# Kernel optimization log

Hardware: AMD Instinct MI355X
Metric: run time of the kernel (lower is better)

Reference implementation:

```python
import jax, jax.numpy as jnp
import numpy as np
from jax import lax

B, SEQ, D, DEPTH = 256, 50, 256, 4
N, K, R = 16, 4, 16  # d_state, d_conv, dt_rank
EPS = 1e-5


def rmsnorm(x, w):
    var = jnp.mean(jnp.square(x), axis=-1, keepdims=True)
    return x * lax.rsqrt(var + EPS) * w


def mamba_mixer(h, in_proj_w, conv_w, conv_b, x_proj_w, dt_proj_w, dt_proj_b, A_log, D_skip, out_proj_w):
    # h: (B, L, D)
    xz = h @ in_proj_w                       # (B, L, 2D)
    x_in, z = jnp.split(xz, 2, axis=-1)      # each (B, L, D)
    # causal depthwise conv1d, kernel K, groups=D
    x_bdl = x_in.transpose(0, 2, 1)          # (B, D, L)
    kern = conv_w[:, None, :]                # (D, 1, K)
    x_c = lax.conv_general_dilated(x_bdl, kern, window_strides=(1,),
                                   padding=[(K - 1, 0)], feature_group_count=D,
                                   dimension_numbers=('NCH', 'OIH', 'NCH'))
    x_c = jax.nn.silu(x_c + conv_b[None, :, None]).transpose(0, 2, 1)  # (B, L, D)
    # input-dependent SSM params
    x_dbl = x_c @ x_proj_w                   # (B, L, R+2N)
    dt = jax.nn.softplus(x_dbl[..., :R] @ dt_proj_w + dt_proj_b)       # (B, L, D)
    Bm = x_dbl[..., R:R + N]                 # (B, L, N)
    Cm = x_dbl[..., R + N:]                  # (B, L, N)
    A = -jnp.exp(A_log)                      # (D, N)
    dA = jnp.exp(dt[..., None] * A)          # (B, L, D, N)
    dBx = (dt * x_c)[..., None] * Bm[:, :, None, :]                    # (B, L, D, N)

    def step(hstate, inp):
        dA_t, dBx_t, C_t = inp
        hstate = dA_t * hstate + dBx_t      # (B, D, N)
        y_t = jnp.einsum('bdn,bn->bd', hstate, C_t)
        return hstate, y_t

    h0 = jnp.zeros((h.shape[0], D, N), dtype=h.dtype)
    xs = (dA.transpose(1, 0, 2, 3), dBx.transpose(1, 0, 2, 3), Cm.transpose(1, 0, 2))
    _, ys = lax.scan(step, h0, xs)           # (L, B, D)
    y = ys.transpose(1, 0, 2) + D_skip * x_c
    y = y * jax.nn.silu(z)
    return y @ out_proj_w                    # (B, L, D)


def setup_inputs() -> dict:
    key = jax.random.key(0)
    ks = jax.random.split(key, 16)
    sc = lambda *s: 0.02
    inp = {
        'x': jax.random.normal(ks[0], (B, SEQ), dtype=jnp.float32),
        'proj_w': jax.random.normal(ks[1], (1, D), dtype=jnp.float32) * 0.5,
        'proj_b': jnp.zeros((D,), dtype=jnp.float32),
        'cls_token': jax.random.normal(ks[2], (1, 1, D), dtype=jnp.float32) * 0.02,
        'pos_embed': jax.random.normal(ks[3], (1, SEQ + 1, D), dtype=jnp.float32) * 0.02,
        'norm_w': jnp.ones((DEPTH, D), dtype=jnp.float32),
        'in_proj_w': jax.random.normal(ks[4], (DEPTH, D, 2 * D), dtype=jnp.float32) * (D ** -0.5),
        'conv_w': jax.random.normal(ks[5], (DEPTH, D, K), dtype=jnp.float32) * 0.3,
        'conv_b': jnp.zeros((DEPTH, D), dtype=jnp.float32),
        'x_proj_w': jax.random.normal(ks[6], (DEPTH, D, R + 2 * N), dtype=jnp.float32) * (D ** -0.5),
        'dt_proj_w': jax.random.normal(ks[7], (DEPTH, R, D), dtype=jnp.float32) * (R ** -0.5),
        'dt_proj_b': jnp.log(jnp.expm1(jnp.full((DEPTH, D), 0.01, dtype=jnp.float32))),
        'A_log': jnp.broadcast_to(jnp.log(jnp.arange(1, N + 1, dtype=jnp.float32)), (DEPTH, D, N)).copy(),
        'D_skip': jnp.ones((DEPTH, D), dtype=jnp.float32),
        'out_proj_w': jax.random.normal(ks[8], (DEPTH, D, D), dtype=jnp.float32) * (D ** -0.5),
        'norm_f_w': jnp.ones((D,), dtype=jnp.float32),
    }
    return inp


def reference(x, proj_w, proj_b, cls_token, pos_embed, norm_w, in_proj_w, conv_w,
              conv_b, x_proj_w, dt_proj_w, dt_proj_b, A_log, D_skip, out_proj_w, norm_f_w):
    # LinearEmbed: (B, SEQ) -> (B, SEQ, 1) -> (B, SEQ, D)
    h = x[..., None] @ proj_w + proj_b
    h = h + pos_embed[:, :-1, :]
    cls = cls_token + pos_embed[:, -1:, :]
    h = jnp.concatenate([jnp.broadcast_to(cls, (h.shape[0], 1, D)), h], axis=1)  # (B, L=51, D)
    residual = None
    for i in range(DEPTH):
        residual = h if residual is None else residual + h
        hn = rmsnorm(residual, norm_w[i])
        h = mamba_mixer(hn, in_proj_w[i], conv_w[i], conv_b[i], x_proj_w[i],
                        dt_proj_w[i], dt_proj_b[i], A_log[i], D_skip[i], out_proj_w[i])
    out = rmsnorm(h, norm_f_w)
    return out[:, 0, :]  # return_type='cls'
```

## Files before the change

### kernel.cpp

```cpp
#include <hip/hip_runtime.h>
#include <math.h>

#define DD 256
#define DEPTH 4
#define XD 48
#define NBLK 16
#define NTHR 256


__device__ __forceinline__ float llc_loadf(const float* p) {
    return __hip_atomic_load(p, __ATOMIC_RELAXED, __HIP_MEMORY_SCOPE_AGENT);
}
__device__ __forceinline__ void llc_storef(float* p, float v) {
    __hip_atomic_store(p, v, __ATOMIC_RELAXED, __HIP_MEMORY_SCOPE_AGENT);
}

__device__ __forceinline__ void grid_bar(unsigned int* cnt, unsigned int target) {
    __syncthreads();
    if (threadIdx.x == 0) {
        __hip_atomic_fetch_add(cnt, 1u, __ATOMIC_RELAXED, __HIP_MEMORY_SCOPE_AGENT);
        while (__hip_atomic_load(cnt, __ATOMIC_RELAXED, __HIP_MEMORY_SCOPE_AGENT) < target)
            __builtin_amdgcn_s_sleep(1);
    }
    __syncthreads();
}

__global__ void netmamba_init(unsigned int* cnt) { *cnt = 0u; }

__global__ __launch_bounds__(NTHR, 1)
void netmamba_persist(const float* __restrict__ cls_token,
                      const float* __restrict__ pos_embed,
                      const float* __restrict__ norm_w,
                      const float* __restrict__ in_proj_w,
                      const float* __restrict__ conv_w,
                      const float* __restrict__ conv_b,
                      const float* __restrict__ x_proj_w,
                      const float* __restrict__ dt_proj_w,
                      const float* __restrict__ dt_proj_b,
                      const float* __restrict__ D_skip,
                      const float* __restrict__ out_proj_w,
                      const float* __restrict__ norm_f_w,
                      float* __restrict__ out,
                      float* __restrict__ ws)
{
    const int tid = threadIdx.x, bid = blockIdx.x;
    float* xc_g = ws;
    float* zv_g = ws + DD;
    float* hv_g = ws + 2 * DD;
    unsigned int* cnt = (unsigned int*)(ws + 1024);

    __shared__ float hn[DD], xcl[DD], yv[DD], xdbl[XD];
    __shared__ float4 partA[32][8];
    __shared__ float4 partB[64][4];
    __shared__ float xp[XD][4];
    __shared__ float red[4];
    __shared__ float rstd_s;

    float res_reg = 0.f;
    unsigned int phase = 0;

    for (int L = 0; L < DEPTH; ++L) {
        float rn;
        if (L == 0) rn = cls_token[tid] + pos_embed[50 * DD + tid];
        else        rn = res_reg + llc_loadf(&hv_g[tid]);
        res_reg = rn;

        float ss = rn * rn;
        #pragma unroll
        for (int o = 32; o > 0; o >>= 1) ss += __shfl_down(ss, o, 64);
        if ((tid & 63) == 0) red[tid >> 6] = ss;
        __syncthreads();
        if (tid == 0)
            rstd_s = rsqrtf((red[0] + red[1] + red[2] + red[3]) * (1.f / DD) + 1e-5f);
        __syncthreads();
        hn[tid] = rn * rstd_s * norm_w[L * DD + tid];
        __syncthreads();

        {
            const float4* W4 = (const float4*)in_proj_w + (size_t)L * DD * 128;
            const int cg = tid & 7, seg = tid >> 3;
            const int col4 = bid * 8 + cg;
            float4 acc = make_float4(0.f, 0.f, 0.f, 0.f);
            #pragma unroll
            for (int i = 0; i < 8; ++i) {
                const int d = seg * 8 + i;
                const float h = hn[d];
                const float4 w = W4[(size_t)d * 128 + col4];
                acc.x += h * w.x; acc.y += h * w.y;
                acc.z += h * w.z; acc.w += h * w.w;
            }
            partA[seg][cg] = acc;
        }
        __syncthreads();
        if (tid < 32) {
            const float* pf = (const float*)partA;
            float s = 0.f;
            #pragma unroll
            for (int g = 0; g < 32; ++g) s += pf[g * 32 + tid];
            const int gc = bid * 32 + tid;
            if (gc < DD) {
                const float pre = conv_w[(L * DD + gc) * 4 + 3] * s + conv_b[L * DD + gc];
                llc_storef(&xc_g[gc], pre / (1.f + __expf(-pre)));
            } else {
                llc_storef(&zv_g[gc - DD], s);
            }
        }
        ++phase;
        grid_bar(cnt, phase * NBLK);

        xcl[tid] = llc_loadf(&xc_g[tid]);
        const float zval = llc_loadf(&zv_g[tid]);
        __syncthreads();

        if (tid < 192) {
            const int j = tid >> 2, q = tid & 3;
            const float* Wx = x_proj_w + (size_t)L * DD * XD;
            float acc = 0.f;
            #pragma unroll 8
            for (int i = 0; i < 64; ++i) {
                const int d = q * 64 + i;
                acc += xcl[d] * Wx[(size_t)d * XD + j];
            }
            xp[j][q] = acc;
        }
        __syncthreads();
        if (tid < XD) xdbl[tid] = xp[tid][0] + xp[tid][1] + xp[tid][2] + xp[tid][3];
        __syncthreads();

        {
            const float* Wdt = dt_proj_w + (size_t)L * 16 * DD;
            float acc = dt_proj_b[L * DD + tid];
            #pragma unroll
            for (int r = 0; r < 16; ++r) acc += xdbl[r] * Wdt[r * DD + tid];
            const float dtv = fmaxf(acc, 0.f) + log1pf(__expf(-fabsf(acc)));
            float sbc = 0.f;
            #pragma unroll
            for (int n = 0; n < 16; ++n) sbc += xdbl[16 + n] * xdbl[32 + n];
            const float y = (dtv * sbc + D_skip[L * DD + tid]) * xcl[tid];
            yv[tid] = y * (zval / (1.f + __expf(-zval)));
        }
        __syncthreads();

        {
            const float4* Wo = (const float4*)out_proj_w + (size_t)L * DD * 64;
            const int c = tid & 3, seg = tid >> 2;
            const int col4 = bid * 4 + c;
            float4 acc = make_float4(0.f, 0.f, 0.f, 0.f);
            #pragma unroll
            for (int i = 0; i < 4; ++i) {
                const int d = seg * 4 + i;
                const float y = yv[d];
                const float4 w = Wo[(size_t)d * 64 + col4];
                acc.x += y * w.x; acc.y += y * w.y;
                acc.z += y * w.z; acc.w += y * w.w;
            }
            partB[seg][c] = acc;
        }
        __syncthreads();
        #pragma unroll
        for (int off = 32; off >= 8; off >>= 1) {
            const int s = tid >> 2, c = tid & 3;
            if (s < off) {
                float4 a = partB[s][c], b = partB[s + off][c];
                a.x += b.x; a.y += b.y; a.z += b.z; a.w += b.w;
                partB[s][c] = a;
            }
            __syncthreads();
        }
        if (tid < 16) {
            const float* pf = (const float*)partB;
            float s = 0.f;
            #pragma unroll
            for (int g = 0; g < 8; ++g) s += pf[g * 16 + tid];
            llc_storef(&hv_g[bid * 16 + tid], s);
        }
        ++phase;
        grid_bar(cnt, phase * NBLK);
    }

    {
        const float x = llc_loadf(&hv_g[tid]);
        float ss = x * x;
        #pragma unroll
        for (int o = 32; o > 0; o >>= 1) ss += __shfl_down(ss, o, 64);
        if ((tid & 63) == 0) red[tid >> 6] = ss;
        __syncthreads();
        if (tid == 0)
            rstd_s = rsqrtf((red[0] + red[1] + red[2] + red[3]) * (1.f / DD) + 1e-5f);
        __syncthreads();
        hn[tid] = x * rstd_s * norm_f_w[tid];
    }
    __syncthreads();
    {
        const float4* o4 = (const float4*)hn;
        float4* out4 = (float4*)out;
        #pragma unroll
        for (int k = 0; k < 4; ++k) {
            const int idx = k * NTHR + tid;
            const int row = bid * 16 + (idx >> 6);
            out4[(size_t)row * 64 + (idx & 63)] = o4[idx & 63];
        }
    }
}

extern "C" void kernel_launch(void* const* d_in, const int* in_sizes, int n_in,
                              void* d_out, int out_size, void* d_ws, size_t ws_size,
                              hipStream_t stream) {
    float* ws = (float*)d_ws;
    unsigned int* cnt = (unsigned int*)(ws + 1024);

    netmamba_init<<<dim3(1), dim3(1), 0, stream>>>(cnt);
    netmamba_persist<<<dim3(NBLK), dim3(NTHR), 0, stream>>>(
        (const float*)d_in[3], (const float*)d_in[4], (const float*)d_in[5],
        (const float*)d_in[6], (const float*)d_in[7], (const float*)d_in[8],
        (const float*)d_in[9], (const float*)d_in[10], (const float*)d_in[11],
        (const float*)d_in[13], (const float*)d_in[14], (const float*)d_in[15],
        (float*)d_out, ws);
}
```

Baseline: 44.11 us.

## Restructure into per-layer dataflow blocks with preloaded weights and point-to-point flags

```diff
diff --git a/kernel.cpp b/kernel.cpp
--- a/kernel.cpp
+++ b/kernel.cpp
@@ -3,10 +3,22 @@
 
 #define DD 256
 #define DEPTH 4
-#define XD 48
-#define NBLK 16
+#define WPG 16
+#define BPG 17
+#define NBLK (DEPTH * BPG)
 #define NTHR 256
 
+#define WS_XC   0
+#define WS_ZV   256
+#define WS_YV   512
+#define WS_HV   1024
+#define WS_FLAG 2048
+
+#define NX_WX   0
+#define NX_WDT  13312
+#define NX_DS   17408
+#define NX_DB   17664
+#define DYN_FLOATS 17920
 
 __device__ __forceinline__ float llc_loadf(const float* p) {
     return __hip_atomic_load(p, __ATOMIC_RELAXED, __HIP_MEMORY_SCOPE_AGENT);
@@ -14,56 +26,103 @@
 __device__ __forceinline__ void llc_storef(float* p, float v) {
     __hip_atomic_store(p, v, __ATOMIC_RELAXED, __HIP_MEMORY_SCOPE_AGENT);
 }
-
-__device__ __forceinline__ void grid_bar(unsigned int* cnt, unsigned int target) {
-    __syncthreads();
-    if (threadIdx.x == 0) {
-        __hip_atomic_fetch_add(cnt, 1u, __ATOMIC_RELAXED, __HIP_MEMORY_SCOPE_AGENT);
-        while (__hip_atomic_load(cnt, __ATOMIC_RELAXED, __HIP_MEMORY_SCOPE_AGENT) < target)
-            __builtin_amdgcn_s_sleep(1);
-    }
-    __syncthreads();
-}
-
-__global__ void netmamba_init(unsigned int* cnt) { *cnt = 0u; }
+__device__ __forceinline__ unsigned llc_loadu(const unsigned* p) {
+    return __hip_atomic_load(p, __ATOMIC_RELAXED, __HIP_MEMORY_SCOPE_AGENT);
+}
+__device__ __forceinline__ void flag_add(unsigned* p) {
+    __hip_atomic_fetch_add(p, 1u, __ATOMIC_RELAXED, __HIP_MEMORY_SCOPE_AGENT);
+}
+
+__global__ void netmamba_init(unsigned* flags) { flags[threadIdx.x] = 0u; }
 
 __global__ __launch_bounds__(NTHR, 1)
-void netmamba_persist(const float* __restrict__ cls_token,
-                      const float* __restrict__ pos_embed,
-                      const float* __restrict__ norm_w,
-                      const float* __restrict__ in_proj_w,
-                      const float* __restrict__ conv_w,
-                      const float* __restrict__ conv_b,
-                      const float* __restrict__ x_proj_w,
-                      const float* __restrict__ dt_proj_w,
-                      const float* __restrict__ dt_proj_b,
-                      const float* __restrict__ D_skip,
-                      const float* __restrict__ out_proj_w,
-                      const float* __restrict__ norm_f_w,
-                      float* __restrict__ out,
-                      float* __restrict__ ws)
+void netmamba_df(const float* __restrict__ cls_token,
+                 const float* __restrict__ pos_embed,
+                 const float* __restrict__ norm_w,
+                 const float* __restrict__ in_proj_w,
+                 const float* __restrict__ conv_w,
+                 const float* __restrict__ conv_b,
+                 const float* __restrict__ x_proj_w,
+                 const float* __restrict__ dt_proj_w,
+                 const float* __restrict__ dt_proj_b,
+                 const float* __restrict__ D_skip,
+                 const float* __restrict__ out_proj_w,
+                 const float* __restrict__ norm_f_w,
+                 float* __restrict__ out,
+                 float* __restrict__ ws)
 {
-    const int tid = threadIdx.x, bid = blockIdx.x;
-    float* xc_g = ws;
-    float* zv_g = ws + DD;
-    float* hv_g = ws + 2 * DD;
-    unsigned int* cnt = (unsigned int*)(ws + 1024);
-
-    __shared__ float hn[DD], xcl[DD], yv[DD], xdbl[XD];
-    __shared__ float4 partA[32][8];
-    __shared__ float4 partB[64][4];
-    __shared__ float xp[XD][4];
+    extern __shared__ float dyn[];
+    const int tid = threadIdx.x;
+    const int bid = blockIdx.x;
+    const int g   = bid / BPG;
+    const int r   = bid % BPG;
+    const bool narrow = (r == WPG);
+
+    float* xc_g = ws + WS_XC;
+    float* zv_g = ws + WS_ZV;
+    float* yv_g = ws + WS_YV;
+    float* hv_g = ws + WS_HV;
+    unsigned* flags = (unsigned*)(ws + WS_FLAG);
+
+    __shared__ float sh_a[DD];
+    __shared__ float sh_b[DD];
+    __shared__ float sh_c[DD];
+    __shared__ float sh_d[64];
     __shared__ float red[4];
     __shared__ float rstd_s;
 
-    float res_reg = 0.f;
-    unsigned int phase = 0;
-
-    for (int L = 0; L < DEPTH; ++L) {
-        float rn;
-        if (L == 0) rn = cls_token[tid] + pos_embed[50 * DD + tid];
-        else        rn = res_reg + llc_loadf(&hv_g[tid]);
-        res_reg = rn;
+    if (!narrow) {
+        const float4* Gi = (const float4*)in_proj_w + (size_t)(g * DD) * 128 + r * 8;
+        float4* Li = (float4*)dyn;
+        #pragma unroll
+        for (int k = 0; k < 8; ++k) {
+            const int m = tid + k * 256;
+            Li[m] = Gi[(size_t)(m >> 3) * 128 + (m & 7)];
+        }
+        const float4* Go = (const float4*)out_proj_w + (size_t)(g * DD) * 64 + r * 4;
+        float4* Lo = (float4*)(dyn + 8192);
+        #pragma unroll
+        for (int k = 0; k < 4; ++k) {
+            const int m = tid + k * 256;
+            Lo[m] = Go[(size_t)(m >> 2) * 64 + (m & 3)];
+        }
+        if (r < 8 && tid < 32) {
+            const int gc = r * 32 + tid;
+            sh_d[tid]      = conv_w[((size_t)g * DD + gc) * 4 + 3];
+            sh_d[32 + tid] = conv_b[g * DD + gc];
+        }
+    } else {
+        const float4* Gx = (const float4*)x_proj_w + (size_t)(g * DD) * 12;
+        #pragma unroll
+        for (int k = 0; k < 12; ++k) {
+            const int m = tid + k * 256;
+            const int d = m / 12, c4 = m % 12;
+            *(float4*)(dyn + NX_WX + d * 52 + c4 * 4) = Gx[(size_t)d * 12 + c4];
+        }
+        const float4* Gd = (const float4*)dt_proj_w + (size_t)g * 1024;
+        float4* Ld = (float4*)(dyn + NX_WDT);
+        #pragma unroll
+        for (int k = 0; k < 4; ++k) { const int m = tid + k * 256; Ld[m] = Gd[m]; }
+        dyn[NX_DS + tid] = D_skip[g * DD + tid];
+        dyn[NX_DB + tid] = dt_proj_b[g * DD + tid];
+    }
+    const float nf_reg = norm_f_w[tid];
+    float iv_reg = 0.f, nw_reg = 0.f;
+    if (!narrow) {
+        iv_reg = cls_token[tid] + pos_embed[50 * DD + tid];
+        nw_reg = norm_w[g * DD + tid];
+    }
+    __syncthreads();
+
+    if (!narrow) {
+        if (g > 0) {
+            if (tid == 0)
+                while (llc_loadu(&flags[(8 + g - 1) * 16]) < WPG)
+                    __builtin_amdgcn_s_sleep(1);
+            __syncthreads();
+        }
+        float rn = iv_reg;
+        for (int l = 0; l < g; ++l) rn += llc_loadf(&hv_g[l * DD + tid]);
 
         float ss = rn * rn;
         #pragma unroll
@@ -73,113 +132,106 @@
         if (tid == 0)
             rstd_s = rsqrtf((red[0] + red[1] + red[2] + red[3]) * (1.f / DD) + 1e-5f);
         __syncthreads();
-        hn[tid] = rn * rstd_s * norm_w[L * DD + tid];
+        sh_a[tid] = rn * rstd_s * nw_reg;
         __syncthreads();
 
         {
-            const float4* W4 = (const float4*)in_proj_w + (size_t)L * DD * 128;
-            const int cg = tid & 7, seg = tid >> 3;
-            const int col4 = bid * 8 + cg;
-            float4 acc = make_float4(0.f, 0.f, 0.f, 0.f);
-            #pragma unroll
-            for (int i = 0; i < 8; ++i) {
-                const int d = seg * 8 + i;
-                const float h = hn[d];
-                const float4 w = W4[(size_t)d * 128 + col4];
-                acc.x += h * w.x; acc.y += h * w.y;
-                acc.z += h * w.z; acc.w += h * w.w;
-            }
-            partA[seg][cg] = acc;
+            const int c = tid & 31, q = tid >> 5;
+            float acc = 0.f;
+            #pragma unroll
+            for (int i = 0; i < 32; ++i) {
+                const int d = q * 32 + i;
+                acc += sh_a[d] * dyn[d * 32 + c];
+            }
+            sh_b[q * 32 + c] = acc;
         }
         __syncthreads();
         if (tid < 32) {
-            const float* pf = (const float*)partA;
             float s = 0.f;
             #pragma unroll
-            for (int g = 0; g < 32; ++g) s += pf[g * 32 + tid];
-            const int gc = bid * 32 + tid;
-            if (gc < DD) {
-                const float pre = conv_w[(L * DD + gc) * 4 + 3] * s + conv_b[L * DD + gc];
+            for (int p = 0; p < 8; ++p) s += sh_b[p * 32 + tid];
+            const int gc = r * 32 + tid;
+            if (r < 8) {
+                const float pre = sh_d[tid] * s + sh_d[32 + tid];
                 llc_storef(&xc_g[gc], pre / (1.f + __expf(-pre)));
             } else {
                 llc_storef(&zv_g[gc - DD], s);
             }
         }
-        ++phase;
-        grid_bar(cnt, phase * NBLK);
-
-        xcl[tid] = llc_loadf(&xc_g[tid]);
-        const float zval = llc_loadf(&zv_g[tid]);
-        __syncthreads();
-
+        __syncthreads();
+        if (tid == 0) flag_add(&flags[g * 16]);
+
+        if (tid == 0)
+            while (llc_loadu(&flags[(4 + g) * 16]) < 1)
+                __builtin_amdgcn_s_sleep(1);
+        __syncthreads();
+        sh_c[tid] = llc_loadf(&yv_g[tid]);
+        __syncthreads();
+        {
+            const int c2 = tid & 15, q2 = tid >> 4;
+            const float* Lo = dyn + 8192;
+            float acc = 0.f;
+            #pragma unroll
+            for (int i = 0; i < 16; ++i) {
+                const int d = i * 16 + q2;
+                acc += sh_c[d] * Lo[d * 16 + c2];
+            }
+            sh_b[q2 * 16 + c2] = acc;
+        }
+        __syncthreads();
+        if (tid < 16) {
+            float s = 0.f;
+            #pragma unroll
+            for (int p = 0; p < 16; ++p) s += sh_b[p * 16 + tid];
+            llc_storef(&hv_g[g * DD + r * 16 + tid], s);
+        }
+        __syncthreads();
+        if (tid == 0) flag_add(&flags[(8 + g) * 16]);
+    } else {
+        if (tid == 0)
+            while (llc_loadu(&flags[g * 16]) < WPG)
+                __builtin_amdgcn_s_sleep(1);
+        __syncthreads();
+        sh_a[tid] = llc_loadf(&xc_g[tid]);
+        sh_b[tid] = llc_loadf(&zv_g[tid]);
+        __syncthreads();
         if (tid < 192) {
             const int j = tid >> 2, q = tid & 3;
-            const float* Wx = x_proj_w + (size_t)L * DD * XD;
             float acc = 0.f;
             #pragma unroll 8
             for (int i = 0; i < 64; ++i) {
-                const int d = q * 64 + i;
-                acc += xcl[d] * Wx[(size_t)d * XD + j];
-            }
-            xp[j][q] = acc;
-        }
-        __syncthreads();
-        if (tid < XD) xdbl[tid] = xp[tid][0] + xp[tid][1] + xp[tid][2] + xp[tid][3];
-        __syncthreads();
-
+                const int d = i * 4 + q;
+                acc += sh_a[d] * dyn[NX_WX + d * 52 + j];
+            }
+            sh_c[j * 4 + q] = acc;
+        }
+        __syncthreads();
+        if (tid < 48)
+            sh_d[tid] = sh_c[tid * 4] + sh_c[tid * 4 + 1] + sh_c[tid * 4 + 2] + sh_c[tid * 4 + 3];
+        __syncthreads();
         {
-            const float* Wdt = dt_proj_w + (size_t)L * 16 * DD;
-            float acc = dt_proj_b[L * DD + tid];
-            #pragma unroll
-            for (int r = 0; r < 16; ++r) acc += xdbl[r] * Wdt[r * DD + tid];
+            const float* Wdt = dyn + NX_WDT;
+            float acc = dyn[NX_DB + tid];
+            #pragma unroll
+            for (int rr = 0; rr < 16; ++rr) acc += sh_d[rr] * Wdt[rr * 256 + tid];
             const float dtv = fmaxf(acc, 0.f) + log1pf(__expf(-fabsf(acc)));
             float sbc = 0.f;
             #pragma unroll
-            for (int n = 0; n < 16; ++n) sbc += xdbl[16 + n] * xdbl[32 + n];
-            const float y = (dtv * sbc + D_skip[L * DD + tid]) * xcl[tid];
-            yv[tid] = y * (zval / (1.f + __expf(-zval)));
-        }
-        __syncthreads();
-
-        {
-            const float4* Wo = (const float4*)out_proj_w + (size_t)L * DD * 64;
-            const int c = tid & 3, seg = tid >> 2;
-            const int col4 = bid * 4 + c;
-            float4 acc = make_float4(0.f, 0.f, 0.f, 0.f);
-            #pragma unroll
-            for (int i = 0; i < 4; ++i) {
-                const int d = seg * 4 + i;
-                const float y = yv[d];
-                const float4 w = Wo[(size_t)d * 64 + col4];
-                acc.x += y * w.x; acc.y += y * w.y;
-                acc.z += y * w.z; acc.w += y * w.w;
-            }
-            partB[seg][c] = acc;
-        }
-        __syncthreads();
-        #pragma unroll
-        for (int off = 32; off >= 8; off >>= 1) {
-            const int s = tid >> 2, c = tid & 3;
-            if (s < off) {
-                float4 a = partB[s][c], b = partB[s + off][c];
-                a.x += b.x; a.y += b.y; a.z += b.z; a.w += b.w;
-                partB[s][c] = a;
-            }
-            __syncthreads();
-        }
-        if (tid < 16) {
-            const float* pf = (const float*)partB;
-            float s = 0.f;
-            #pragma unroll
-            for (int g = 0; g < 8; ++g) s += pf[g * 16 + tid];
-            llc_storef(&hv_g[bid * 16 + tid], s);
-        }
-        ++phase;
-        grid_bar(cnt, phase * NBLK);
-    }
-
+            for (int n = 0; n < 16; ++n) sbc += sh_d[16 + n] * sh_d[32 + n];
+            const float y = (dtv * sbc + dyn[NX_DS + tid]) * sh_a[tid];
+            const float z = sh_b[tid];
+            llc_storef(&yv_g[tid], y * (z / (1.f + __expf(-z))));
+        }
+        __syncthreads();
+        if (tid == 0) flag_add(&flags[(4 + g) * 16]);
+    }
+
+    if (tid == 0)
+        while (llc_loadu(&flags[(8 + 3) * 16]) < WPG)
+            __builtin_amdgcn_s_sleep(1);
+    __syncthreads();
     {
-        const float x = llc_loadf(&hv_g[tid]);
+        const float x = llc_loadf(&hv_g[3 * DD + tid]);
         float ss = x * x;
         #pragma unroll
         for (int o = 32; o > 0; o >>= 1) ss += __shfl_down(ss, o, 64);
@@ -188,18 +240,15 @@
         if (tid == 0)
             rstd_s = rsqrtf((red[0] + red[1] + red[2] + red[3]) * (1.f / DD) + 1e-5f);
         __syncthreads();
-        hn[tid] = x * rstd_s * norm_f_w[tid];
+        sh_a[tid] = x * rstd_s * nf_reg;
     }
     __syncthreads();
-    {
-        const float4* o4 = (const float4*)hn;
-        float4* out4 = (float4*)out;
-        #pragma unroll
-        for (int k = 0; k < 4; ++k) {
-            const int idx = k * NTHR + tid;
-            const int row = bid * 16 + (idx >> 6);
-            out4[(size_t)row * 64 + (idx & 63)] = o4[idx & 63];
-        }
+    if (bid < 64) {
+        const int row = bid * 4 + (tid >> 6);
+        const int cc  = tid & 63;
+        const float4 v = make_float4(sh_a[cc * 4], sh_a[cc * 4 + 1],
+                                     sh_a[cc * 4 + 2], sh_a[cc * 4 + 3]);
+        ((float4*)out)[(size_t)row * 64 + cc] = v;
     }
 }
 
@@ -207,10 +256,10 @@
                               void* d_out, int out_size, void* d_ws, size_t ws_size,
                               hipStream_t stream) {
     float* ws = (float*)d_ws;
-    unsigned int* cnt = (unsigned int*)(ws + 1024);
-
-    netmamba_init<<<dim3(1), dim3(1), 0, stream>>>(cnt);
-    netmamba_persist<<<dim3(NBLK), dim3(NTHR), 0, stream>>>(
+    unsigned* flags = (unsigned*)(ws + WS_FLAG);
+
+    netmamba_init<<<dim3(1), dim3(256), 0, stream>>>(flags);
+    netmamba_df<<<dim3(NBLK), dim3(NTHR), DYN_FLOATS * sizeof(float), stream>>>(
         (const float*)d_in[3], (const float*)d_in[4], (const float*)d_in[5],
         (const float*)d_in[6], (const float*)d_in[7], (const float*)d_in[8],
         (const float*)d_in[9], (const float*)d_in[10], (const float*)d_in[11],
```

Measured after the change: 43.93 us. About the same (-0.4%).
